# Optimization experiments

Measured on AMD Instinct MI355X. Metric: run time of the kernel, lower is better.

The kernel has to match this reference:

```python
import jax, jax.numpy as jnp
import numpy as np
import math

SEQ_LEN = 2048
DIM = 4096
N_HEADS = 32
N_KV_HEADS = 8
HEAD_DIM = DIM // N_HEADS  # 128
ROPE_THETA = 500000.0
W_SCALE = 0.02


def _precompute_freqs(head_dim, end, theta=ROPE_THETA):
    freq = 1.0 / theta ** (jnp.arange(0, head_dim, 2, dtype=jnp.float32) / head_dim)  # [hd/2]
    t = jnp.arange(end, dtype=jnp.float32)
    f = t[:, None] * freq[None, :]  # [S, hd/2]
    return jnp.cos(f), jnp.sin(f)


def _apply_rope(x, cos, sin):
    # x: [S, H, hd]; interleaved even/odd rotation, matching torch ::2 / 1::2 indexing
    xe = x[:, :, 0::2]
    xo = x[:, :, 1::2]
    c = cos[:, None, :]  # [S, 1, hd/2]
    s = sin[:, None, :]
    re = xe * c - xo * s
    ro = xe * s + xo * c
    # re-interleave: out[..., 2i] = re[..., i], out[..., 2i+1] = ro[..., i]
    return jnp.stack([re, ro], axis=-1).reshape(x.shape)


def setup_inputs() -> dict:
    key = jax.random.key(0)
    k = jax.random.split(key, 5)
    x = jax.random.normal(k[0], (SEQ_LEN, DIM), dtype=jnp.float32)
    wq = jax.random.normal(k[1], (DIM, DIM), dtype=jnp.float32) * W_SCALE
    wk = jax.random.normal(k[2], (N_KV_HEADS * HEAD_DIM, DIM), dtype=jnp.float32) * W_SCALE
    wv = jax.random.normal(k[3], (N_KV_HEADS * HEAD_DIM, DIM), dtype=jnp.float32) * W_SCALE
    wo = jax.random.normal(k[4], (DIM, DIM), dtype=jnp.float32) * W_SCALE
    return {"x": x, "wq": wq, "wk": wk, "wv": wv, "wo": wo}


def reference(x, wq, wk, wv, wo):
    S = SEQ_LEN
    rep = N_HEADS // N_KV_HEADS  # 4

    Q = (x @ wq.T).reshape(S, N_HEADS, HEAD_DIM)
    K = (x @ wk.T).reshape(S, N_KV_HEADS, HEAD_DIM)
    V = (x @ wv.T).reshape(S, N_KV_HEADS, HEAD_DIM)

    cos, sin = _precompute_freqs(HEAD_DIM, S)
    Q = _apply_rope(Q, cos, sin)
    K = _apply_rope(K, cos, sin)

    # GQA: repeat_interleave(K, rep, dim=1) maps query head h -> kv group h // rep.
    # Express natively with a grouped einsum instead of materializing repeated K/V.
    Qg = Q.transpose(1, 0, 2).reshape(N_KV_HEADS, rep, S, HEAD_DIM)  # [g, r, S, d]
    Kt = K.transpose(1, 0, 2)  # [g, S, d]
    Vt = V.transpose(1, 0, 2)  # [g, S, d]

    scores = jnp.einsum('grqd,gkd->grqk', Qg, Kt) / math.sqrt(HEAD_DIM)
    mask = jnp.triu(jnp.full((S, S), -jnp.inf, dtype=scores.dtype), k=1)
    probs = jax.nn.softmax(scores + mask, axis=-1)
    out = jnp.einsum('grqk,gkd->grqd', probs, Vt)  # [g, r, S, d]

    out = out.reshape(N_HEADS, S, HEAD_DIM).transpose(1, 0, 2).reshape(S, N_HEADS * HEAD_DIM)
    return out @ wo.T
```

## Files before the change

### kernel.cpp

```cpp
#include <hip/hip_runtime.h>

typedef unsigned short u16;
typedef short short8 __attribute__((ext_vector_type(8)));
typedef float f32x4 __attribute__((ext_vector_type(4)));
typedef unsigned short u16x4 __attribute__((ext_vector_type(4)));

typedef short8 short8_a __attribute__((may_alias));
typedef f32x4 f32x4_a __attribute__((may_alias));
typedef u16x4 u16x4_a __attribute__((may_alias));
typedef unsigned int uint_a __attribute__((may_alias));

__device__ __forceinline__ u16 f2b(float f) {
  unsigned u = __float_as_uint(f);
  u += 0x7FFFu + ((u >> 16) & 1u);
  return (u16)(u >> 16);
}

__device__ __forceinline__ void mfma_b(f32x4& d, short8 a, short8 b) {
  asm("v_mfma_f32_16x16x32_bf16 %0, %1, %2, %0" : "+v"(d) : "v"(a), "v"(b));
}

__device__ __forceinline__ void guard4(f32x4& a, f32x4& b, f32x4& c, f32x4& d) {
  asm volatile("s_nop 7\n\ts_nop 7" : "+v"(a), "+v"(b), "+v"(c), "+v"(d));
}
__device__ __forceinline__ void guard8(f32x4* o) {
  asm volatile("s_nop 7\n\ts_nop 7"
               : "+v"(o[0]), "+v"(o[1]), "+v"(o[2]), "+v"(o[3]),
                 "+v"(o[4]), "+v"(o[5]), "+v"(o[6]), "+v"(o[7]));
}

__device__ __forceinline__ void gload16(const void* g, void* l) {
  __builtin_amdgcn_global_load_lds((__attribute__((address_space(1))) void*)(g),
                                   (__attribute__((address_space(3))) void*)(l),
                                   16, 0, 0);
}

__global__ __launch_bounds__(256) void k_cast(const float* __restrict__ in,
                                              u16* __restrict__ out, int n4) {
  int i = blockIdx.x * 256 + threadIdx.x;
  if (i >= n4) return;
  f32x4 v = ((const f32x4_a*)in)[i];
  u16x4 o;
  o[0] = f2b(v[0]); o[1] = f2b(v[1]); o[2] = f2b(v[2]); o[3] = f2b(v[3]);
  ((u16x4_a*)out)[i] = o;
}

__global__ __launch_bounds__(256) void k_tab(float* __restrict__ cost,
                                             float* __restrict__ sint) {
  int i = blockIdx.x * 256 + threadIdx.x;
  int s = i >> 6, j = i & 63;
  float freq = powf(500000.0f, -(float)j * (1.0f / 64.0f));
  float a = (float)s * freq;
  float sv, cv;
  sincosf(a, &sv, &cv);
  cost[i] = cv;
  sint[i] = sv;
}

#define QK_SCALE 0.08838834764831845f
template <int EPI>
__global__ __launch_bounds__(256, 2)
void k_gemm_t(const u16* __restrict__ A, const u16* __restrict__ B,
              float* __restrict__ C, int M, int N, int K,
              const float* __restrict__ cost, const float* __restrict__ sint,
              u16* __restrict__ Qb, u16* __restrict__ Kb, u16* __restrict__ Vt) {
  __shared__ u16 As[2][4096];
  __shared__ u16 Bs[2][4096];
  const int tid = threadIdx.x;
  const int w = tid >> 6, lane = tid & 63;
  const int hi = lane >> 4, lo = lane & 15;
  const int nwg = gridDim.x;
  int bid = blockIdx.x;
  if ((nwg & 7) == 0) bid = (bid & 7) * (nwg >> 3) + (bid >> 3);
  const int ntn = N >> 7;
  const int tm = bid / ntn, tn = bid - tm * ntn;
  const int m0 = tm << 7, n0 = tn << 7;
  const int wr = w >> 1, wc = w & 1;

  const int e0 = w * 512 + lane * 8;
  const int e1 = e0 + 2048;
  const u16* Ag0 = A + (long)(m0 + (e0 >> 5)) * K + (e0 & 31);
  const u16* Ag1 = A + (long)(m0 + (e1 >> 5)) * K + (e1 & 31);
  const u16* Bg0 = B + (long)(n0 + (e0 >> 5)) * K + (e0 & 31);
  const u16* Bg1 = B + (long)(n0 + (e1 >> 5)) * K + (e1 & 31);
  const int sb = w * 512;

  f32x4 acc[4][4] = {};
  const int aoff = (wr * 64 + lo) * 32 + hi * 8;
  const int boff = (wc * 64 + lo) * 32 + hi * 8;

  const int nt = K >> 5;
  int cur = 0;
  gload16(Ag0, &As[0][sb]);
  gload16(Ag1, &As[0][sb + 2048]);
  gload16(Bg0, &Bs[0][sb]);
  gload16(Bg1, &Bs[0][sb + 2048]);
  __syncthreads();
  for (int t = 0; t < nt; ++t) {
    if (t + 1 < nt) {
      const int k0 = (t + 1) << 5;
      const int nx = cur ^ 1;
      gload16(Ag0 + k0, &As[nx][sb]);
      gload16(Ag1 + k0, &As[nx][sb + 2048]);
      gload16(Bg0 + k0, &Bs[nx][sb]);
      gload16(Bg1 + k0, &Bs[nx][sb + 2048]);
    }
    short8 af[4], bf[4];
#pragma unroll
    for (int m = 0; m < 4; ++m) af[m] = *(const short8_a*)(&As[cur][aoff + m * 512]);
#pragma unroll
    for (int n = 0; n < 4; ++n) bf[n] = *(const short8_a*)(&Bs[cur][boff + n * 512]);
#pragma unroll
    for (int m = 0; m < 4; ++m)
#pragma unroll
      for (int n = 0; n < 4; ++n) mfma_b(acc[m][n], af[m], bf[n]);
    __syncthreads();
    cur ^= 1;
  }
  guard8(&acc[0][0]);
  guard8(&acc[2][0]);

  if constexpr (EPI == 0) {
#pragma unroll
    for (int m = 0; m < 4; ++m) {
      const int row0 = m0 + wr * 64 + m * 16 + hi * 4;
#pragma unroll
      for (int n = 0; n < 4; ++n) {
        const int col = n0 + wc * 64 + n * 16 + lo;
#pragma unroll
        for (int r = 0; r < 4; ++r)
          C[(long)(row0 + r) * N + col] = acc[m][n][r];
      }
    }
  } else {
    if (n0 < 5120) {
      const bool isQ = (n0 < 4096);
#pragma unroll
      for (int m = 0; m < 4; ++m) {
        const int row0 = m0 + wr * 64 + m * 16 + hi * 4;
#pragma unroll
        for (int n = 0; n < 4; ++n) {
          const int c = n0 + wc * 64 + n * 16 + lo;
          const int j0 = (c & 127) >> 1;
          const bool even = ((c & 1) == 0);
#pragma unroll
          for (int r = 0; r < 4; ++r) {
            float own = acc[m][n][r];
            float part = __shfl_xor(own, 1);
            const int s_ = row0 + r;
            const float cv = cost[s_ * 64 + j0];
            const float sv = sint[s_ * 64 + j0];
            float res = even ? (own * cv - part * sv) : (part * sv + own * cv);
            if (isQ)
              Qb[(long)s_ * 4096 + c] = f2b(res * QK_SCALE);
            else
              Kb[(long)s_ * 1024 + (c - 4096)] = f2b(res);
          }
        }
      }
    } else {
#pragma unroll
      for (int m = 0; m < 4; ++m) {
        const int row0 = m0 + wr * 64 + m * 16 + hi * 4;
#pragma unroll
        for (int n = 0; n < 4; ++n) {
          const int vc = n0 - 5120 + wc * 64 + n * 16 + lo;
          u16x4 pk;
#pragma unroll
          for (int r = 0; r < 4; ++r) pk[r] = f2b(acc[m][n][r]);
          *(u16x4_a*)(Vt + (long)vc * 2048 + row0) = pk;
        }
      }
    }
  }
}

#define KLD 136
#define VLD 72
__global__ __launch_bounds__(256, 2)
void k_attn(const u16* __restrict__ Qb, const u16* __restrict__ Kb,
            const u16* __restrict__ Vt, u16* __restrict__ Ab) {
  __shared__ u16 Ks[64 * KLD];
  __shared__ u16 Vs[128 * VLD];
  __shared__ u16 Ps[4 * 16 * VLD];

  const int tid = threadIdx.x;
  const int w = tid >> 6, lane = tid & 63;
  const int hi = lane >> 4, lo = lane & 15;
  const int qt = 31 - (blockIdx.x >> 5);
  const int h = blockIdx.x & 31;
  const int hkv = h >> 2;
  const int q0 = qt * 64;
  const int qrow = q0 + w * 16 + lo;

  short8 qf[4];
#pragma unroll
  for (int c = 0; c < 4; ++c)
    qf[c] = *(const short8_a*)(Qb + (long)qrow * 4096 + h * 128 + c * 32 + hi * 8);

  f32x4 o[8] = {};
  float m_run = -1e30f, l_run = 0.f;
  u16* Pw = Ps + w * (16 * VLD);

  const int ntiles = qt + 1;
  for (int t = 0; t < ntiles; ++t) {
    const int kv0 = t * 64;
    __syncthreads();
#pragma unroll
    for (int r = 0; r < 4; ++r) {
      int i = r * 256 + tid;
      int key = i >> 4, d8 = (i & 15) * 8;
      short8 v = *(const short8_a*)(Kb + (long)(kv0 + key) * 1024 + hkv * 128 + d8);
      *(short8_a*)(Ks + key * KLD + d8) = v;
    }
#pragma unroll
    for (int r = 0; r < 4; ++r) {
      int i = r * 256 + tid;
      int dd = i >> 3, k8 = (i & 7) * 8;
      short8 v = *(const short8_a*)(Vt + (long)hkv * 262144 + (long)dd * 2048 + kv0 + k8);
      *(short8_a*)(Vs + dd * VLD + k8) = v;
    }
    __syncthreads();

    f32x4 sc[4] = {};
#pragma unroll
    for (int c = 0; c < 4; ++c) {
#pragma unroll
      for (int kt = 0; kt < 4; ++kt) {
        short8 kf = *(const short8_a*)(Ks + (kt * 16 + lo) * KLD + c * 32 + hi * 8);
        mfma_b(sc[kt], kf, qf[c]);
      }
    }
    guard4(sc[0], sc[1], sc[2], sc[3]);

    if (t == ntiles - 1) {
#pragma unroll
      for (int kt = 0; kt < 4; ++kt)
#pragma unroll
        for (int r = 0; r < 4; ++r) {
          int key = kv0 + kt * 16 + hi * 4 + r;
          if (key > qrow) sc[kt][r] = -1e30f;
        }
    }
    float tmax = -1e30f;
#pragma unroll
    for (int kt = 0; kt < 4; ++kt)
#pragma unroll
      for (int r = 0; r < 4; ++r) tmax = fmaxf(tmax, sc[kt][r]);
    tmax = fmaxf(tmax, __shfl_xor(tmax, 16));
    tmax = fmaxf(tmax, __shfl_xor(tmax, 32));
    float m_new = fmaxf(m_run, tmax);
    float scale = __expf(m_run - m_new);
    float psum = 0.f;
    float p[16];
#pragma unroll
    for (int kt = 0; kt < 4; ++kt)
#pragma unroll
      for (int r = 0; r < 4; ++r) {
        float pv = __expf(sc[kt][r] - m_new);
        p[kt * 4 + r] = pv;
        psum += pv;
      }
    psum += __shfl_xor(psum, 16);
    psum += __shfl_xor(psum, 32);
    l_run = l_run * scale + psum;
    m_run = m_new;
    float srow[4];
#pragma unroll
    for (int r = 0; r < 4; ++r) srow[r] = __shfl(scale, hi * 4 + r);
#pragma unroll
    for (int n = 0; n < 8; ++n)
#pragma unroll
      for (int r = 0; r < 4; ++r) o[n][r] *= srow[r];
#pragma unroll
    for (int kt = 0; kt < 4; ++kt) {
      unsigned p01 = (unsigned)f2b(p[kt * 4]) | ((unsigned)f2b(p[kt * 4 + 1]) << 16);
      unsigned p23 = (unsigned)f2b(p[kt * 4 + 2]) | ((unsigned)f2b(p[kt * 4 + 3]) << 16);
      *(uint_a*)(Pw + lo * VLD + kt * 16 + hi * 4) = p01;
      *(uint_a*)(Pw + lo * VLD + kt * 16 + hi * 4 + 2) = p23;
    }
    __syncthreads();
#pragma unroll
    for (int c = 0; c < 2; ++c) {
      short8 pf = *(const short8_a*)(Pw + lo * VLD + c * 32 + hi * 8);
#pragma unroll
      for (int n = 0; n < 8; ++n) {
        short8 vf = *(const short8_a*)(Vs + (n * 16 + lo) * VLD + c * 32 + hi * 8);
        mfma_b(o[n], pf, vf);
      }
    }
  }
  guard8(o);

  float inv = 1.0f / l_run;
  float irow[4];
#pragma unroll
  for (int r = 0; r < 4; ++r) irow[r] = __shfl(inv, hi * 4 + r);
#pragma unroll
  for (int n = 0; n < 8; ++n)
#pragma unroll
    for (int r = 0; r < 4; ++r) {
      int q = q0 + w * 16 + hi * 4 + r;
      Ab[(long)q * 4096 + h * 128 + n * 16 + lo] = f2b(o[n][r] * irow[r]);
    }
}

extern "C" void kernel_launch(void* const* d_in, const int* in_sizes, int n_in,
                              void* d_out, int out_size, void* d_ws, size_t ws_size,
                              hipStream_t stream) {
  const float* x = (const float*)d_in[0];
  const float* wq = (const float*)d_in[1];
  const float* wk = (const float*)d_in[2];
  const float* wv = (const float*)d_in[3];
  const float* wo = (const float*)d_in[4];
  float* out = (float*)d_out;
  char* ws = (char*)d_ws;

  size_t off = 0;
  u16* xb = (u16*)(ws + off); off += 16777216;
  u16* wB = (u16*)(ws + off); off += 50331648;
  u16* wob = (u16*)(ws + off); off += 33554432;
  u16* Qb = (u16*)(ws + off); off += 16777216;
  u16* Kb = (u16*)(ws + off); off += 4194304;
  u16* Vtb = (u16*)(ws + off); off += 4194304;
  float* cost = (float*)(ws + off); off += 524288;
  float* sint = (float*)(ws + off); off += 524288;
  u16* Ab = (u16*)(ws + off); off += 16777216;

  k_cast<<<8192, 256, 0, stream>>>(x, xb, 2097152);
  k_cast<<<16384, 256, 0, stream>>>(wq, wB, 4194304);
  k_cast<<<4096, 256, 0, stream>>>(wk, wB + 16777216, 1048576);
  k_cast<<<4096, 256, 0, stream>>>(wv, wB + 20971520, 1048576);
  k_cast<<<16384, 256, 0, stream>>>(wo, wob, 4194304);
  k_tab<<<512, 256, 0, stream>>>(cost, sint);

  k_gemm_t<1><<<768, 256, 0, stream>>>(xb, wB, nullptr, 2048, 6144, 4096,
                                       cost, sint, Qb, Kb, Vtb);

  k_attn<<<1024, 256, 0, stream>>>(Qb, Kb, Vtb, Ab);

  k_gemm_t<0><<<512, 256, 0, stream>>>(Ab, wob, out, 2048, 4096, 4096,
                                       nullptr, nullptr, nullptr, nullptr, nullptr);
}
```

Before: 385.6 us.

## Triple-buffer GEMM LDS loads with swizzle and fuse prep casts into one kernel

```diff
diff --git a/kernel.cpp b/kernel.cpp
--- a/kernel.cpp
+++ b/kernel.cpp
@@ -35,26 +35,46 @@
                                    16, 0, 0);
 }
 
-__global__ __launch_bounds__(256) void k_cast(const float* __restrict__ in,
-                                              u16* __restrict__ out, int n4) {
-  int i = blockIdx.x * 256 + threadIdx.x;
-  if (i >= n4) return;
-  f32x4 v = ((const f32x4_a*)in)[i];
+__device__ __forceinline__ void bar_v4() {
+  asm volatile("s_waitcnt vmcnt(4)\n\ts_barrier" ::: "memory");
+}
+__device__ __forceinline__ void bar_v0() {
+  asm volatile("s_waitcnt vmcnt(0)\n\ts_barrier" ::: "memory");
+}
+
+__global__ __launch_bounds__(256)
+void k_prep(const float* __restrict__ x, const float* __restrict__ wq,
+            const float* __restrict__ wk, const float* __restrict__ wv,
+            const float* __restrict__ wo, u16* __restrict__ xb,
+            u16* __restrict__ wB, u16* __restrict__ wob,
+            float* __restrict__ cost, float* __restrict__ sint) {
+  const long i = (long)blockIdx.x * 256 + threadIdx.x;
+  const float* src;
+  u16* dst;
+  long j;
+  if (i < 6291456) {
+    if (i < 2097152) { src = x; dst = xb; j = i; }
+    else { src = wq; dst = wB; j = i - 2097152; }
+  } else if (i < 8388608) {
+    if (i < 7340032) { src = wk; dst = wB + 16777216; j = i - 6291456; }
+    else { src = wv; dst = wB + 20971520; j = i - 7340032; }
+  } else if (i < 12582912) {
+    src = wo; dst = wob; j = i - 8388608;
+  } else {
+    long ti = i - 12582912;
+    int s = (int)(ti >> 6), jj = (int)(ti & 63);
+    float freq = powf(500000.0f, -(float)jj * (1.0f / 64.0f));
+    float a = (float)s * freq;
+    float sv, cv;
+    sincosf(a, &sv, &cv);
+    cost[ti] = cv;
+    sint[ti] = sv;
+    return;
+  }
+  f32x4 v = ((const f32x4_a*)src)[j];
   u16x4 o;
   o[0] = f2b(v[0]); o[1] = f2b(v[1]); o[2] = f2b(v[2]); o[3] = f2b(v[3]);
-  ((u16x4_a*)out)[i] = o;
-}
-
-__global__ __launch_bounds__(256) void k_tab(float* __restrict__ cost,
-                                             float* __restrict__ sint) {
-  int i = blockIdx.x * 256 + threadIdx.x;
-  int s = i >> 6, j = i & 63;
-  float freq = powf(500000.0f, -(float)j * (1.0f / 64.0f));
-  float a = (float)s * freq;
-  float sv, cv;
-  sincosf(a, &sv, &cv);
-  cost[i] = cv;
-  sint[i] = sv;
+  ((u16x4_a*)dst)[j] = o;
 }
 
 #define QK_SCALE 0.08838834764831845f
@@ -64,8 +84,8 @@
               float* __restrict__ C, int M, int N, int K,
               const float* __restrict__ cost, const float* __restrict__ sint,
               u16* __restrict__ Qb, u16* __restrict__ Kb, u16* __restrict__ Vt) {
-  __shared__ u16 As[2][4096];
-  __shared__ u16 Bs[2][4096];
+  __shared__ u16 As[12288];
+  __shared__ u16 Bs[12288];
   const int tid = threadIdx.x;
   const int w = tid >> 6, lane = tid & 63;
   const int hi = lane >> 4, lo = lane & 15;
@@ -77,45 +97,52 @@
   const int m0 = tm << 7, n0 = tn << 7;
   const int wr = w >> 1, wc = w & 1;
 
-  const int e0 = w * 512 + lane * 8;
-  const int e1 = e0 + 2048;
-  const u16* Ag0 = A + (long)(m0 + (e0 >> 5)) * K + (e0 & 31);
-  const u16* Ag1 = A + (long)(m0 + (e1 >> 5)) * K + (e1 & 31);
-  const u16* Bg0 = B + (long)(n0 + (e0 >> 5)) * K + (e0 & 31);
-  const u16* Bg1 = B + (long)(n0 + (e1 >> 5)) * K + (e1 & 31);
+  const int rowl = w * 16 + (lane >> 2);
+  const int ks = (((lane & 3) ^ ((lane >> 3) & 3)) << 3);
+  const u16* Ag0 = A + (long)(m0 + rowl) * K + ks;
+  const u16* Ag1 = A + (long)(m0 + 64 + rowl) * K + ks;
+  const u16* Bg0 = B + (long)(n0 + rowl) * K + ks;
+  const u16* Bg1 = B + (long)(n0 + 64 + rowl) * K + ks;
   const int sb = w * 512;
 
   f32x4 acc[4][4] = {};
-  const int aoff = (wr * 64 + lo) * 32 + hi * 8;
-  const int boff = (wc * 64 + lo) * 32 + hi * 8;
+  const int hs = hi ^ ((lo >> 1) & 3);
+  const int aoff = (wr * 64 + lo) * 32 + hs * 8;
+  const int boff = (wc * 64 + lo) * 32 + hs * 8;
 
   const int nt = K >> 5;
-  int cur = 0;
-  gload16(Ag0, &As[0][sb]);
-  gload16(Ag1, &As[0][sb + 2048]);
-  gload16(Bg0, &Bs[0][sb]);
-  gload16(Bg1, &Bs[0][sb + 2048]);
-  __syncthreads();
+  int c0 = 0, c1 = 4096, c2 = 8192;
+
+  gload16(Ag0, As + c0 + sb);       gload16(Ag1, As + c0 + sb + 2048);
+  gload16(Bg0, Bs + c0 + sb);       gload16(Bg1, Bs + c0 + sb + 2048);
+  gload16(Ag0 + 32, As + c1 + sb);  gload16(Ag1 + 32, As + c1 + sb + 2048);
+  gload16(Bg0 + 32, Bs + c1 + sb);  gload16(Bg1 + 32, Bs + c1 + sb + 2048);
+  bar_v4();
+
   for (int t = 0; t < nt; ++t) {
-    if (t + 1 < nt) {
-      const int k0 = (t + 1) << 5;
-      const int nx = cur ^ 1;
-      gload16(Ag0 + k0, &As[nx][sb]);
-      gload16(Ag1 + k0, &As[nx][sb + 2048]);
-      gload16(Bg0 + k0, &Bs[nx][sb]);
-      gload16(Bg1 + k0, &Bs[nx][sb + 2048]);
+    if (t + 2 < nt) {
+      const int k0 = (t + 2) << 5;
+      gload16(Ag0 + k0, As + c2 + sb);
+      gload16(Ag1 + k0, As + c2 + sb + 2048);
+      gload16(Bg0 + k0, Bs + c2 + sb);
+      gload16(Bg1 + k0, Bs + c2 + sb + 2048);
     }
     short8 af[4], bf[4];
 #pragma unroll
-    for (int m = 0; m < 4; ++m) af[m] = *(const short8_a*)(&As[cur][aoff + m * 512]);
-#pragma unroll
-    for (int n = 0; n < 4; ++n) bf[n] = *(const short8_a*)(&Bs[cur][boff + n * 512]);
-#pragma unroll
     for (int m = 0; m < 4; ++m)
+      af[m] = *(const short8_a*)(As + c0 + aoff + m * 512);
+#pragma unroll
+    for (int n = 0; n < 4; ++n)
+      bf[n] = *(const short8_a*)(Bs + c0 + boff + n * 512);
+    __builtin_amdgcn_s_setprio(1);
+#pragma unroll
+    for (int m = 0; m < 4; ++m)
 #pragma unroll
       for (int n = 0; n < 4; ++n) mfma_b(acc[m][n], af[m], bf[n]);
-    __syncthreads();
-    cur ^= 1;
+    __builtin_amdgcn_s_setprio(0);
+    if (t + 2 < nt) bar_v4();
+    else bar_v0();
+    const int tmp = c0; c0 = c1; c1 = c2; c2 = tmp;
   }
   guard8(&acc[0][0]);
   guard8(&acc[2][0]);
@@ -327,12 +354,7 @@
   float* sint = (float*)(ws + off); off += 524288;
   u16* Ab = (u16*)(ws + off); off += 16777216;
 
-  k_cast<<<8192, 256, 0, stream>>>(x, xb, 2097152);
-  k_cast<<<16384, 256, 0, stream>>>(wq, wB, 4194304);
-  k_cast<<<4096, 256, 0, stream>>>(wk, wB + 16777216, 1048576);
-  k_cast<<<4096, 256, 0, stream>>>(wv, wB + 20971520, 1048576);
-  k_cast<<<16384, 256, 0, stream>>>(wo, wob, 4194304);
-  k_tab<<<512, 256, 0, stream>>>(cost, sint);
+  k_prep<<<49664, 256, 0, stream>>>(x, wq, wk, wv, wo, xb, wB, wob, cost, sint);
 
   k_gemm_t<1><<<768, 256, 0, stream>>>(xb, wB, nullptr, 2048, 6144, 4096,
                                        cost, sint, Qb, Kb, Vtb);
```

Measured after the change: 378.3 us. No clear change (-1.9%).
